# Kernel optimization log

Measured on AMD Instinct MI355X. Metric: run time of the kernel, lower is better.

The kernel has to match this reference:

```python
import jax, jax.numpy as jnp
import numpy as np
from math import sqrt

B, L, D_MODEL = 4, 128, 256
V, D_WORD = 50257, 768
H = 8  # n_heads; d_keys = D_MODEL // H = 32


def setup_inputs() -> dict:
    key = jax.random.key(0)
    ks = jax.random.split(key, 10)
    s = lambda k, shape, fan: jax.random.normal(k, shape, dtype=jnp.float32) / np.sqrt(fan)
    return {
        "time_series_embedding": jax.random.normal(ks[0], (B, L, D_MODEL), dtype=jnp.float32),
        "word_embedding": jax.random.normal(ks[1], (V, D_WORD), dtype=jnp.float32) * 0.02,
        "Wq": s(ks[2], (D_MODEL, D_MODEL), D_MODEL),
        "bq": jnp.zeros((D_MODEL,), jnp.float32),
        "Wk": s(ks[3], (D_WORD, D_MODEL), D_WORD),
        "bk": jnp.zeros((D_MODEL,), jnp.float32),
        "Wv": s(ks[4], (D_WORD, D_MODEL), D_WORD),
        "bv": jnp.zeros((D_MODEL,), jnp.float32),
        "Wo": s(ks[5], (D_MODEL, D_MODEL), D_MODEL),
        "bo": jnp.zeros((D_MODEL,), jnp.float32),
    }


def reference(time_series_embedding, word_embedding, Wq, bq, Wk, bk, Wv, bv, Wo, bo):
    b, l, _ = time_series_embedding.shape
    v, _ = word_embedding.shape
    h = H
    e = D_MODEL // h
    # projections
    query = (time_series_embedding @ Wq + bq).reshape(b, l, h, e)   # [B,L,H,E]
    key = (word_embedding @ Wk + bk).reshape(v, h, e)               # [V,H,E]
    value = (word_embedding @ Wv + bv).reshape(v, h, e)             # [V,H,E]
    scale = 1.0 / sqrt(e)
    # scores over full vocab: [B,H,V,L]
    scores = jnp.einsum('blhe,vhe->bhvl', query, key)
    # NOTE: faithful to source -- softmax over the LAST axis (l, the query dim)
    attn = jax.nn.softmax(scale * scores, axis=-1)
    # dropout is identity in eval mode
    reprog = jnp.einsum('bhvl,vhe->blhe', attn, value).reshape(b, l, h * e)
    return reprog @ Wo + bo  # [B,L,d_model]
```

## Files before the change

kernel.cpp:

```cpp
#include <hip/hip_runtime.h>
#include <hip/hip_bf16.h>
#include <string.h>

#define BB 4
#define LL 128
#define DM 256
#define VV 50257
#define VPAD 50304
#define DW 768
#define HH 8
#define EE 32

typedef __attribute__((ext_vector_type(8))) short sh8;
typedef __attribute__((ext_vector_type(4))) short sh4;
typedef __attribute__((ext_vector_type(4))) float f32x4;

static __device__ inline unsigned short bfbits(float x) {
  __hip_bfloat16 h = __float2bfloat16(x);
  unsigned short u;
  __builtin_memcpy(&u, &h, 2);
  return u;
}

#define GLDS16(gsrc, ldst)                                                    \
  __builtin_amdgcn_global_load_lds(                                          \
      (const __attribute__((address_space(1))) void*)(gsrc),                 \
      (__attribute__((address_space(3))) void*)(ldst), 16, 0, 0)

#define WAIT_VM(N)                                                           \
  __builtin_amdgcn_sched_barrier(0);                                         \
  asm volatile("s_waitcnt vmcnt(" #N ")" ::: "memory");                      \
  __builtin_amdgcn_sched_barrier(0)
#define WAIT_LGKM0                                                           \
  asm volatile("s_waitcnt lgkmcnt(0)" ::: "memory");                         \
  __builtin_amdgcn_sched_barrier(0)
#define SBARRIER                                                             \
  __builtin_amdgcn_sched_barrier(0);                                         \
  __builtin_amdgcn_s_barrier();                                              \
  __builtin_amdgcn_sched_barrier(0)

#if __has_builtin(__builtin_amdgcn_mfma_f32_16x16x16bf16_1k)
#define MFMA16(A, B, C) __builtin_amdgcn_mfma_f32_16x16x16bf16_1k(A, B, C, 0, 0, 0)
#elif __has_builtin(__builtin_amdgcn_mfma_f32_16x16x16_bf16)
#define MFMA16(A, B, C) __builtin_amdgcn_mfma_f32_16x16x16_bf16(A, B, C, 0, 0, 0)
#else
static __device__ inline f32x4 mfma16_asm(sh4 a, sh4 b, f32x4 c) {
  asm volatile("v_mfma_f32_16x16x16_bf16 %0, %1, %2, %0"
               : "+v"(c) : "v"(a), "v"(b));
  return c;
}
#define MFMA16(A, B, C) mfma16_asm(A, B, C)
#endif

__global__ __launch_bounds__(256) void prep_kernel(
    const float* __restrict__ Wk, const float* __restrict__ Wv,
    unsigned short* __restrict__ Wkt, unsigned short* __restrict__ Wvt,
    const float* __restrict__ tse, const float* __restrict__ Wq,
    const float* __restrict__ bq, unsigned short* __restrict__ Qb) {
  __shared__ float tileS[64][65];
  int bid = blockIdx.x;
  int t = threadIdx.x;
  if (bid < 96) {
    int z = bid / 48, rem = bid - z * 48;
    int x = rem % 12, y = rem / 12;
    const float* src = z ? Wv : Wk;
    unsigned short* dst = z ? Wvt : Wkt;
    int k0 = x * 64, n0 = y * 64;
    int c = t & 63, rb = t >> 6;
#pragma unroll
    for (int j = 0; j < 16; ++j) {
      int r = j * 4 + rb;
      tileS[r][c] = src[(size_t)(k0 + r) * DM + n0 + c];
    }
    __syncthreads();
#pragma unroll
    for (int j = 0; j < 16; ++j) {
      int r = j * 4 + rb;
      dst[(size_t)(n0 + r) * DW + k0 + c] = bfbits(tileS[c][r]);
    }
  } else {
    int r = bid - 96;
    int n = t;
    float* row = &tileS[0][0];
    row[n] = tse[r * DM + n];
    __syncthreads();
    float acc = bq[n];
#pragma unroll 8
    for (int k = 0; k < DM; ++k)
      acc = fmaf(row[k], Wq[k * DM + n], acc);
    const float scale = 0.17677669529663687f * 1.4426950408889634f;
    Qb[r * DM + n] = bfbits(acc * scale);
  }
}

__global__ __launch_bounds__(256, 2) void kvproj_kernel(
    const float* __restrict__ WE, const unsigned short* __restrict__ Wkt,
    const unsigned short* __restrict__ Wvt, const float* __restrict__ bk,
    const float* __restrict__ bv, unsigned short* __restrict__ Kb,
    unsigned short* __restrict__ Vbt) {
  __shared__ float WEf[2][128 * 32];
  __shared__ short Kbuf[2][128 * 32];
  __shared__ short Vbuf[2][128 * 32];

  int bx = blockIdx.x;
  int v0 = (bx >> 1) * 128;
  int colbase = (bx & 1) * 128;
  int t = threadIdx.x;
  int w = t >> 6, lane = t & 63, a = lane & 15, quad = lane >> 4;
  int wm = w >> 1, wn = w & 1;

  auto stage = [&](int kt, int p) {
#pragma unroll
    for (int i = 0; i < 4; ++i) {
      int s = w * 256 + i * 64 + lane;
      int row = s >> 3;
      int cc = (s & 7) ^ (row & 7);
      int grow = v0 + row;
      if (grow > VV - 1) grow = VV - 1;
      GLDS16(WE + (size_t)grow * DW + kt * 32 + cc * 4,
             &WEf[p][(w * 256 + i * 64) * 4]);
    }
#pragma unroll
    for (int i = 0; i < 2; ++i) {
      int s = w * 128 + i * 64 + lane;
      int row = s >> 2;
      int cc = (s & 3) ^ ((row >> 1) & 3);
      GLDS16(Wkt + (size_t)(colbase + row) * DW + kt * 32 + cc * 8,
             &Kbuf[p][(w * 128 + i * 64) * 8]);
      GLDS16(Wvt + (size_t)(colbase + row) * DW + kt * 32 + cc * 8,
             &Vbuf[p][(w * 128 + i * 64) * 8]);
    }
  };

  f32x4 Ck[4][4], Cv[4][4];
#pragma unroll
  for (int mb = 0; mb < 4; ++mb)
#pragma unroll
    for (int nb = 0; nb < 4; ++nb) {
      Ck[mb][nb] = (f32x4){0.f, 0.f, 0.f, 0.f};
      Cv[mb][nb] = (f32x4){0.f, 0.f, 0.f, 0.f};
    }

  stage(0, 0);
  stage(1, 1);

  for (int kt = 0; kt < 24; ++kt) {
    int p = kt & 1;
    if (kt < 23) {
      WAIT_VM(8);
    } else {
      WAIT_VM(0);
    }
    SBARRIER;

    sh8 A[4], Bk[4], Bv[4];
#pragma unroll
    for (int mb = 0; mb < 4; ++mb) {
      int row = wm * 64 + mb * 16 + a;
      const float* rp = &WEf[p][row * 32];
      f32x4 lo = *(const f32x4*)(rp + ((2 * quad) ^ (a & 7)) * 4);
      f32x4 hi = *(const f32x4*)(rp + ((2 * quad + 1) ^ (a & 7)) * 4);
      sh4 l4 = {(short)bfbits(lo[0]), (short)bfbits(lo[1]),
                (short)bfbits(lo[2]), (short)bfbits(lo[3])};
      sh4 h4 = {(short)bfbits(hi[0]), (short)bfbits(hi[1]),
                (short)bfbits(hi[2]), (short)bfbits(hi[3])};
      A[mb] = __builtin_shufflevector(l4, h4, 0, 1, 2, 3, 4, 5, 6, 7);
    }
#pragma unroll
    for (int nb = 0; nb < 4; ++nb) {
      int krow = (wn * 4 + nb) * 16 + a;
      int cp = (quad ^ ((krow >> 1) & 3)) * 8;
      Bk[nb] = *(const sh8*)&Kbuf[p][krow * 32 + cp];
      Bv[nb] = *(const sh8*)&Vbuf[p][krow * 32 + cp];
    }
#pragma unroll
    for (int mb = 0; mb < 4; ++mb)
#pragma unroll
      for (int nb = 0; nb < 4; ++nb) {
        Ck[mb][nb] = __builtin_amdgcn_mfma_f32_16x16x32_bf16(
            A[mb], Bk[nb], Ck[mb][nb], 0, 0, 0);
        Cv[mb][nb] = __builtin_amdgcn_mfma_f32_16x16x32_bf16(
            A[mb], Bv[nb], Cv[mb][nb], 0, 0, 0);
      }

    WAIT_LGKM0;
    SBARRIER;
    if (kt < 22) stage(kt + 2, p);
  }

  float bkv[4], bvv[4];
#pragma unroll
  for (int nb = 0; nb < 4; ++nb) {
    int n = colbase + (wn * 4 + nb) * 16 + a;
    bkv[nb] = bk[n];
    bvv[nb] = bv[n];
  }
#pragma unroll
  for (int mb = 0; mb < 4; ++mb)
#pragma unroll
    for (int nb = 0; nb < 4; ++nb) {
      int m0 = v0 + wm * 64 + mb * 16 + quad * 4;
      int n = colbase + (wn * 4 + nb) * 16 + a;
      sh4 vq;
#pragma unroll
      for (int r = 0; r < 4; ++r) {
        int m = m0 + r;
        bool ok = m < VV;
        Kb[(size_t)m * DM + n] = ok ? bfbits(Ck[mb][nb][r] + bkv[nb]) : 0;
        vq[r] = ok ? (short)bfbits(Cv[mb][nb][r] + bvv[nb]) : (short)0;
      }
      *(sh4*)&Vbt[(size_t)n * VPAD + m0] = vq;
    }
}

__global__ __launch_bounds__(256) void attn_kernel(
    const unsigned short* __restrict__ Qb, const unsigned short* __restrict__ Kb,
    const unsigned short* __restrict__ Vbt, float* __restrict__ part, int bpb,
    int nc) {
  __shared__ float Cred[4][32][129];

  int bh = blockIdx.x / bpb;
  int chunk = blockIdx.x - bh * bpb;
  int b = bh >> 3, h = bh & 7;
  int t = threadIdx.x;
  int w = t >> 6;
  int lane = t & 63;
  int a = lane & 15;
  int quad = lane >> 4;

  sh8 qf[8];
  const unsigned short* qbase = Qb + (size_t)(b * LL) * DM + h * EE;
#pragma unroll
  for (int tau = 0; tau < 8; ++tau)
    qf[tau] = *(const sh8*)(qbase + (size_t)(tau * 16 + a) * DM + quad * 8);

  f32x4 C2[2][8];
#pragma unroll
  for (int nb = 0; nb < 2; ++nb)
#pragma unroll
    for (int tau = 0; tau < 8; ++tau)
      C2[nb][tau] = (f32x4){0.f, 0.f, 0.f, 0.f};

  const int ntiles = VPAD >> 6;

  sh8 af;
  sh4 av[2];
  {
    int v0 = chunk << 6;
    af = *(const sh8*)(Kb + (size_t)(v0 + 16 * w + a) * DM + h * EE + quad * 8);
#pragma unroll
    for (int nb = 0; nb < 2; ++nb)
      av[nb] = *(const sh4*)(Vbt + (size_t)(h * EE + nb * 16 + a) * VPAD +
                             v0 + 16 * w + quad * 4);
  }

  for (int tile = chunk; tile < ntiles; tile += bpb) {
    f32x4 S[8];
#pragma unroll
    for (int tau = 0; tau < 8; ++tau) {
      f32x4 z = {0.f, 0.f, 0.f, 0.f};
      S[tau] = __builtin_amdgcn_mfma_f32_16x16x32_bf16(af, qf[tau], z, 0, 0, 0);
    }

    sh8 af2 = af;
    sh4 av2[2] = {av[0], av[1]};
    int nt = tile + bpb;
    if (nt < ntiles) {
      int v0n = nt << 6;
      af2 = *(const sh8*)(Kb + (size_t)(v0n + 16 * w + a) * DM + h * EE + quad * 8);
#pragma unroll
      for (int nb = 0; nb < 2; ++nb)
        av2[nb] = *(const sh4*)(Vbt + (size_t)(h * EE + nb * 16 + a) * VPAD +
                                v0n + 16 * w + quad * 4);
    }

    float sm[4], inv[4];
#pragma unroll
    for (int r = 0; r < 4; ++r) sm[r] = 0.f;
#pragma unroll
    for (int tau = 0; tau < 8; ++tau)
#pragma unroll
      for (int r = 0; r < 4; ++r) {
        float ex = __builtin_amdgcn_exp2f(S[tau][r]);
        S[tau][r] = ex;
        sm[r] += ex;
      }
#pragma unroll
    for (int msk = 1; msk <= 8; msk <<= 1)
#pragma unroll
      for (int r = 0; r < 4; ++r)
        sm[r] += __shfl_xor(sm[r], msk);
#pragma unroll
    for (int r = 0; r < 4; ++r) inv[r] = 1.f / sm[r];

    sh4 pb[8];
#pragma unroll
    for (int tau = 0; tau < 8; ++tau) {
      pb[tau][0] = (short)bfbits(S[tau][0] * inv[0]);
      pb[tau][1] = (short)bfbits(S[tau][1] * inv[1]);
      pb[tau][2] = (short)bfbits(S[tau][2] * inv[2]);
      pb[tau][3] = (short)bfbits(S[tau][3] * inv[3]);
    }

#pragma unroll
    for (int nb = 0; nb < 2; ++nb)
#pragma unroll
      for (int tau = 0; tau < 8; ++tau)
        C2[nb][tau] = MFMA16(av[nb], pb[tau], C2[nb][tau]);

    af = af2;
    av[0] = av2[0];
    av[1] = av2[1];
  }

#pragma unroll
  for (int nb = 0; nb < 2; ++nb)
#pragma unroll
    for (int tau = 0; tau < 8; ++tau)
#pragma unroll
      for (int r = 0; r < 4; ++r)
        Cred[w][nb * 16 + quad * 4 + r][tau * 16 + a] = C2[nb][tau][r];
  __syncthreads();
#pragma unroll
  for (int j = 0; j < 16; ++j) {
    int f = t + 256 * j;
    int e = f & 31, l = f >> 5;
    float s = Cred[0][e][l] + Cred[1][e][l] + Cred[2][e][l] + Cred[3][e][l];
    size_t idx = (size_t)(b * LL + l) * DM + h * EE + e;
    if (nc > 1)
      part[(size_t)chunk * (BB * LL * DM) + idx] = s;
    else
      atomicAdd(&part[idx], s);
  }
}

__global__ __launch_bounds__(256) void outproj_kernel(
    const float* __restrict__ part, const float* __restrict__ Wo,
    const float* __restrict__ bo, float* __restrict__ out, int nc) {
  __shared__ float row[DM];
  int r = blockIdx.x, n = threadIdx.x;
  float s = 0.f;
  for (int c = 0; c < nc; ++c)
    s += part[(size_t)c * (BB * LL * DM) + (size_t)r * DM + n];
  row[n] = s;
  __syncthreads();
  float acc = bo[n];
#pragma unroll 8
  for (int k = 0; k < DM; ++k)
    acc = fmaf(row[k], Wo[k * DM + n], acc);
  out[r * DM + n] = acc;
}

extern "C" void kernel_launch(void* const* d_in, const int* in_sizes, int n_in,
                              void* d_out, int out_size, void* d_ws, size_t ws_size,
                              hipStream_t stream) {
  const float* tse = (const float*)d_in[0];
  const float* WE  = (const float*)d_in[1];
  const float* Wq  = (const float*)d_in[2];
  const float* bq  = (const float*)d_in[3];
  const float* Wk  = (const float*)d_in[4];
  const float* bk  = (const float*)d_in[5];
  const float* Wv  = (const float*)d_in[6];
  const float* bv  = (const float*)d_in[7];
  const float* Wo  = (const float*)d_in[8];
  const float* bo  = (const float*)d_in[9];
  float* out = (float*)d_out;

  char* ws = (char*)d_ws;
  const size_t QB_BYTES   = (size_t)BB * LL * DM * 2;
  const size_t KV_BYTES   = (size_t)VPAD * DM * 2;
  const size_t WT_BYTES   = (size_t)DM * DW * 2;
  const size_t PART_BYTES = (size_t)BB * LL * DM * 4;
  unsigned short* Qb  = (unsigned short*)ws;
  unsigned short* Kb  = (unsigned short*)(ws + QB_BYTES);
  unsigned short* Vbt = (unsigned short*)(ws + QB_BYTES + KV_BYTES);
  char* X = ws + QB_BYTES + 2 * KV_BYTES;
  unsigned short* Wkt = (unsigned short*)X;
  unsigned short* Wvt = (unsigned short*)(X + WT_BYTES);
  float* part = (float*)X;

  const int BPB = 32;

  const size_t NEED_PART =
      QB_BYTES + 2 * KV_BYTES + (size_t)BPB * PART_BYTES;
  const int nc = (ws_size >= NEED_PART) ? BPB : 1;

  prep_kernel<<<96 + BB * LL, 256, 0, stream>>>(Wk, Wv, Wkt, Wvt, tse, Wq, bq, Qb);
  kvproj_kernel<<<(VPAD / 128) * 2, 256, 0, stream>>>(WE, Wkt, Wvt, bk, bv, Kb, Vbt);
  if (nc == 1)
    (void)hipMemsetAsync(part, 0, PART_BYTES, stream);
  attn_kernel<<<32 * BPB, 256, 0, stream>>>(Qb, Kb, Vbt, part, BPB, nc);
  outproj_kernel<<<BB * LL, 256, 0, stream>>>(part, Wo, bo, out, nc);
}
```

Baseline: 408.7 us.

## Pre-convert word embedding to tiled bf16 and use 16x16x32 MFMA KV projection

The prep kernel gains extra blocks that convert the fp32 word embedding into a bf16 layout tiled by 32-column k-slices. A new KV projection kernel then streams those bf16 tiles straight into LDS with swizzling and uses 16x16x32 bf16 MFMAs at higher occupancy. This is meant to cut LDS footprint and conversion work inside the GEMM, at the cost of an extra full read and write of the embedding matrix. The attention reduction also shrinks its LDS buffer by having half the waves accumulate into the other half's slots, which adds one extra barrier.

```diff
diff --git a/kernel.cpp b/kernel.cpp
--- a/kernel.cpp
+++ b/kernel.cpp
@@ -56,7 +56,8 @@
     const float* __restrict__ Wk, const float* __restrict__ Wv,
     unsigned short* __restrict__ Wkt, unsigned short* __restrict__ Wvt,
     const float* __restrict__ tse, const float* __restrict__ Wq,
-    const float* __restrict__ bq, unsigned short* __restrict__ Qb) {
+    const float* __restrict__ bq, unsigned short* __restrict__ Qb,
+    const float* __restrict__ WE, unsigned short* __restrict__ WEbt) {
   __shared__ float tileS[64][65];
   int bid = blockIdx.x;
   int t = threadIdx.x;
@@ -78,7 +79,7 @@
       int r = j * 4 + rb;
       dst[(size_t)(n0 + r) * DW + k0 + c] = bfbits(tileS[c][r]);
     }
-  } else {
+  } else if (bid < 608) {
     int r = bid - 96;
     int n = t;
     float* row = &tileS[0][0];
@@ -90,10 +91,135 @@
       acc = fmaf(row[k], Wq[k * DM + n], acc);
     const float scale = 0.17677669529663687f * 1.4426950408889634f;
     Qb[r * DM + n] = bfbits(acc * scale);
-  }
-}
-
-__global__ __launch_bounds__(256, 2) void kvproj_kernel(
+  } else {
+    int v0 = (bid - 608) * 64;
+    int c4 = (t & 7) * 4;
+    int r0 = t >> 3;
+#pragma unroll 4
+    for (int kt = 0; kt < 24; ++kt)
+#pragma unroll
+      for (int g = 0; g < 2; ++g) {
+        int row = v0 + g * 32 + r0;
+        sh4 o = {0, 0, 0, 0};
+        if (row < VV) {
+          f32x4 f = *(const f32x4*)(WE + (size_t)row * DW + kt * 32 + c4);
+          o[0] = (short)bfbits(f[0]);
+          o[1] = (short)bfbits(f[1]);
+          o[2] = (short)bfbits(f[2]);
+          o[3] = (short)bfbits(f[3]);
+        }
+        *(sh4*)&WEbt[((size_t)kt * VPAD + row) * 32 + c4] = o;
+      }
+  }
+}
+
+__global__ __launch_bounds__(256, 3) void kvproj_bf16t(
+    const unsigned short* __restrict__ WEbt, const unsigned short* __restrict__ Wkt,
+    const unsigned short* __restrict__ Wvt, const float* __restrict__ bk,
+    const float* __restrict__ bv, unsigned short* __restrict__ Kb,
+    unsigned short* __restrict__ Vbt) {
+  __shared__ short WEb[2][128 * 32];
+  __shared__ short Kbuf[2][128 * 32];
+  __shared__ short Vbuf[2][128 * 32];
+
+  int bx = blockIdx.x;
+  int v0 = (bx >> 1) * 128;
+  int colbase = (bx & 1) * 128;
+  int t = threadIdx.x;
+  int w = t >> 6, lane = t & 63, a = lane & 15, quad = lane >> 4;
+  int wm = w >> 1, wn = w & 1;
+
+  auto stage = [&](int kt, int p) {
+#pragma unroll
+    for (int i = 0; i < 2; ++i) {
+      int s = w * 128 + i * 64 + lane;
+      int row = s >> 2;
+      int cc = (s & 3) ^ ((row >> 1) & 3);
+      GLDS16(WEbt + ((size_t)kt * VPAD + v0 + row) * 32 + cc * 8,
+             &WEb[p][(w * 128 + i * 64) * 8]);
+      GLDS16(Wkt + (size_t)(colbase + row) * DW + kt * 32 + cc * 8,
+             &Kbuf[p][(w * 128 + i * 64) * 8]);
+      GLDS16(Wvt + (size_t)(colbase + row) * DW + kt * 32 + cc * 8,
+             &Vbuf[p][(w * 128 + i * 64) * 8]);
+    }
+  };
+
+  f32x4 Ck[4][4], Cv[4][4];
+#pragma unroll
+  for (int mb = 0; mb < 4; ++mb)
+#pragma unroll
+    for (int nb = 0; nb < 4; ++nb) {
+      Ck[mb][nb] = (f32x4){0.f, 0.f, 0.f, 0.f};
+      Cv[mb][nb] = (f32x4){0.f, 0.f, 0.f, 0.f};
+    }
+
+  stage(0, 0);
+  stage(1, 1);
+
+  for (int kt = 0; kt < 24; ++kt) {
+    int p = kt & 1;
+    if (kt < 23) {
+      WAIT_VM(6);
+    } else {
+      WAIT_VM(0);
+    }
+    SBARRIER;
+
+    sh8 A[4], Bk[4], Bv[4];
+#pragma unroll
+    for (int mb = 0; mb < 4; ++mb) {
+      int row = wm * 64 + mb * 16 + a;
+      int cp = (quad ^ ((row >> 1) & 3)) * 8;
+      A[mb] = *(const sh8*)&WEb[p][row * 32 + cp];
+    }
+#pragma unroll
+    for (int nb = 0; nb < 4; ++nb) {
+      int krow = (wn * 4 + nb) * 16 + a;
+      int cp = (quad ^ ((krow >> 1) & 3)) * 8;
+      Bk[nb] = *(const sh8*)&Kbuf[p][krow * 32 + cp];
+      Bv[nb] = *(const sh8*)&Vbuf[p][krow * 32 + cp];
+    }
+#pragma unroll
+    for (int mb = 0; mb < 4; ++mb)
+#pragma unroll
+      for (int nb = 0; nb < 4; ++nb) {
+        Ck[mb][nb] = __builtin_amdgcn_mfma_f32_16x16x32_bf16(
+            A[mb], Bk[nb], Ck[mb][nb], 0, 0, 0);
+        Cv[mb][nb] = __builtin_amdgcn_mfma_f32_16x16x32_bf16(
+            A[mb], Bv[nb], Cv[mb][nb], 0, 0, 0);
+      }
+
+    WAIT_LGKM0;
+    SBARRIER;
+    if (kt < 22) stage(kt + 2, p);
+  }
+
+  float bkv[4], bvv[4];
+#pragma unroll
+  for (int nb = 0; nb < 4; ++nb) {
+    int n = colbase + (wn * 4 + nb) * 16 + a;
+    bkv[nb] = bk[n];
+    bvv[nb] = bv[n];
+  }
+#pragma unroll
+  for (int mb = 0; mb < 4; ++mb)
+#pragma unroll
+    for (int nb = 0; nb < 4; ++nb) {
+      int m0 = v0 + wm * 64 + mb * 16 + quad * 4;
+      int n = colbase + (wn * 4 + nb) * 16 + a;
+      sh4 vq;
+#pragma unroll
+      for (int r = 0; r < 4; ++r) {
+        int m = m0 + r;
+        bool ok = m < VV;
+        Kb[(size_t)m * DM + n] = ok ? bfbits(Ck[mb][nb][r] + bkv[nb]) : 0;
+        vq[r] = ok ? (short)bfbits(Cv[mb][nb][r] + bvv[nb]) : (short)0;
+      }
+      *(sh4*)&Vbt[(size_t)n * VPAD + m0] = vq;
+    }
+}
+
+__global__ __launch_bounds__(256, 2) void kvproj_fp32(
     const float* __restrict__ WE, const unsigned short* __restrict__ Wkt,
     const unsigned short* __restrict__ Wvt, const float* __restrict__ bk,
     const float* __restrict__ bv, unsigned short* __restrict__ Kb,
@@ -217,7 +343,7 @@
     const unsigned short* __restrict__ Qb, const unsigned short* __restrict__ Kb,
     const unsigned short* __restrict__ Vbt, float* __restrict__ part, int bpb,
     int nc) {
-  __shared__ float Cred[4][32][129];
+  __shared__ float Cred[2][32][129];
 
   int bh = blockIdx.x / bpb;
   int chunk = blockIdx.x - bh * bpb;
@@ -313,19 +439,31 @@
     av[1] = av2[1];
   }
 
-#pragma unroll
-  for (int nb = 0; nb < 2; ++nb)
-#pragma unroll
-    for (int tau = 0; tau < 8; ++tau)
-#pragma unroll
-      for (int r = 0; r < 4; ++r)
-        Cred[w][nb * 16 + quad * 4 + r][tau * 16 + a] = C2[nb][tau][r];
+  if (w < 2) {
+#pragma unroll
+    for (int nb = 0; nb < 2; ++nb)
+#pragma unroll
+      for (int tau = 0; tau < 8; ++tau)
+#pragma unroll
+        for (int r = 0; r < 4; ++r)
+          Cred[w][nb * 16 + quad * 4 + r][tau * 16 + a] = C2[nb][tau][r];
+  }
+  __syncthreads();
+  if (w >= 2) {
+#pragma unroll
+    for (int nb = 0; nb < 2; ++nb)
+#pragma unroll
+      for (int tau = 0; tau < 8; ++tau)
+#pragma unroll
+        for (int r = 0; r < 4; ++r)
+          Cred[w - 2][nb * 16 + quad * 4 + r][tau * 16 + a] += C2[nb][tau][r];
+  }
   __syncthreads();
 #pragma unroll
   for (int j = 0; j < 16; ++j) {
     int f = t + 256 * j;
     int e = f & 31, l = f >> 5;
-    float s = Cred[0][e][l] + Cred[1][e][l] + Cred[2][e][l] + Cred[3][e][l];
+    float s = Cred[0][e][l] + Cred[1][e][l];
     size_t idx = (size_t)(b * LL + l) * DM + h * EE + e;
     if (nc > 1)
       part[(size_t)chunk * (BB * LL * DM) + idx] = s;
@@ -370,23 +508,33 @@
   const size_t QB_BYTES   = (size_t)BB * LL * DM * 2;
   const size_t KV_BYTES   = (size_t)VPAD * DM * 2;
   const size_t WT_BYTES   = (size_t)DM * DW * 2;
+  const size_t WEBT_BYTES = (size_t)VPAD * DW * 2;
   const size_t PART_BYTES = (size_t)BB * LL * DM * 4;
   unsigned short* Qb  = (unsigned short*)ws;
   unsigned short* Kb  = (unsigned short*)(ws + QB_BYTES);
   unsigned short* Vbt = (unsigned short*)(ws + QB_BYTES + KV_BYTES);
   char* X = ws + QB_BYTES + 2 * KV_BYTES;
-  unsigned short* Wkt = (unsigned short*)X;
-  unsigned short* Wvt = (unsigned short*)(X + WT_BYTES);
+  unsigned short* Wkt  = (unsigned short*)X;
+  unsigned short* Wvt  = (unsigned short*)(X + WT_BYTES);
+  unsigned short* WEbt = (unsigned short*)(X + 2 * WT_BYTES);
   float* part = (float*)X;
 
   const int BPB = 32;
 
-  const size_t NEED_PART =
-      QB_BYTES + 2 * KV_BYTES + (size_t)BPB * PART_BYTES;
+  const size_t BASE = QB_BYTES + 2 * KV_BYTES;
+  const size_t NEED_TILED = BASE + 2 * WT_BYTES + WEBT_BYTES;
+  const size_t NEED_PART  = BASE + (size_t)BPB * PART_BYTES;
+  const bool tiled = (ws_size >= NEED_TILED);
   const int nc = (ws_size >= NEED_PART) ? BPB : 1;
 
-  prep_kernel<<<96 + BB * LL, 256, 0, stream>>>(Wk, Wv, Wkt, Wvt, tse, Wq, bq, Qb);
-  kvproj_kernel<<<(VPAD / 128) * 2, 256, 0, stream>>>(WE, Wkt, Wvt, bk, bv, Kb, Vbt);
+  prep_kernel<<<tiled ? 1394 : 608, 256, 0, stream>>>(
+      Wk, Wv, Wkt, Wvt, tse, Wq, bq, Qb, WE, WEbt);
+  if (tiled)
+    kvproj_bf16t<<<(VPAD / 128) * 2, 256, 0, stream>>>(WEbt, Wkt, Wvt, bk, bv,
+                                                       Kb, Vbt);
+  else
+    kvproj_fp32<<<(VPAD / 128) * 2, 256, 0, stream>>>(WE, Wkt, Wvt, bk, bv,
+                                                      Kb, Vbt);
   if (nc == 1)
     (void)hipMemsetAsync(part, 0, PART_BYTES, stream);
   attn_kernel<<<32 * BPB, 256, 0, stream>>>(Qb, Kb, Vbt, part, BPB, nc);
```

Measured after the change: 554.0 us. 35.6% more time.

## Split kvproj WE tile into half-buffers and halve attn reduction LDS

Applied to the files above, without the earlier changes.

The kvproj kernel now stages the fp32 word-embedding tile as two 64-row halves instead of a double-buffered 128-row tile. The first half's MFMAs overlap the load of the second half, and the next step's first half is prefetched while the second half computes. This cuts LDS use so occupancy can rise to 3 blocks per CU, traded against tighter waits and more barriers per k-step. Separately, the attention kernel's cross-wave reduction buffer shrinks from 4 to 2 slices by adding in place in two phases, which lowers LDS footprint at the cost of an extra barrier.

```diff
diff --git a/kernel.cpp b/kernel.cpp
--- a/kernel.cpp
+++ b/kernel.cpp
@@ -93,12 +93,12 @@
   }
 }
 
-__global__ __launch_bounds__(256, 2) void kvproj_kernel(
+__global__ __launch_bounds__(256, 3) void kvproj_kernel(
     const float* __restrict__ WE, const unsigned short* __restrict__ Wkt,
     const unsigned short* __restrict__ Wvt, const float* __restrict__ bk,
     const float* __restrict__ bv, unsigned short* __restrict__ Kb,
     unsigned short* __restrict__ Vbt) {
-  __shared__ float WEf[2][128 * 32];
+  __shared__ float WEh[2][64 * 32];
   __shared__ short Kbuf[2][128 * 32];
   __shared__ short Vbuf[2][128 * 32];
 
@@ -109,26 +109,29 @@
   int w = t >> 6, lane = t & 63, a = lane & 15, quad = lane >> 4;
   int wm = w >> 1, wn = w & 1;
 
-  auto stage = [&](int kt, int p) {
-#pragma unroll
-    for (int i = 0; i < 4; ++i) {
-      int s = w * 256 + i * 64 + lane;
-      int row = s >> 3;
-      int cc = (s & 7) ^ (row & 7);
-      int grow = v0 + row;
+  auto stageWEh = [&](int kt, int h) {
+#pragma unroll
+    for (int i = 0; i < 2; ++i) {
+      int s = w * 128 + i * 64 + lane;
+      int rho = s >> 3;
+      int cc = (s & 7) ^ (rho & 7);
+      int g = (rho < 32) ? (h * 32 + rho) : (64 + h * 32 + (rho - 32));
+      int grow = v0 + g;
       if (grow > VV - 1) grow = VV - 1;
       GLDS16(WE + (size_t)grow * DW + kt * 32 + cc * 4,
-             &WEf[p][(w * 256 + i * 64) * 4]);
-    }
+             &WEh[h][(w * 128 + i * 64) * 4]);
+    }
+  };
+  auto stageKV = [&](int kt, int pb) {
 #pragma unroll
     for (int i = 0; i < 2; ++i) {
       int s = w * 128 + i * 64 + lane;
       int row = s >> 2;
       int cc = (s & 3) ^ ((row >> 1) & 3);
       GLDS16(Wkt + (size_t)(colbase + row) * DW + kt * 32 + cc * 8,
-             &Kbuf[p][(w * 128 + i * 64) * 8]);
+             &Kbuf[pb][(w * 128 + i * 64) * 8]);
       GLDS16(Wvt + (size_t)(colbase + row) * DW + kt * 32 + cc * 8,
-             &Vbuf[p][(w * 128 + i * 64) * 8]);
+             &Vbuf[pb][(w * 128 + i * 64) * 8]);
     }
   };
 
@@ -141,51 +144,85 @@
       Cv[mb][nb] = (f32x4){0.f, 0.f, 0.f, 0.f};
     }
 
-  stage(0, 0);
-  stage(1, 1);
+  stageWEh(0, 0);
+  stageKV(0, 0);
+  stageWEh(0, 1);
+  stageKV(1, 1);
 
   for (int kt = 0; kt < 24; ++kt) {
-    int p = kt & 1;
-    if (kt < 23) {
-      WAIT_VM(8);
+    int pb = kt & 1;
+
+    if (kt == 0) {
+      WAIT_VM(6);
     } else {
       WAIT_VM(0);
     }
     SBARRIER;
-
-    sh8 A[4], Bk[4], Bv[4];
-#pragma unroll
-    for (int mb = 0; mb < 4; ++mb) {
-      int row = wm * 64 + mb * 16 + a;
-      const float* rp = &WEf[p][row * 32];
+    if (kt > 0) stageWEh(kt, 1);
+
+    sh8 A0[2], Bk[4], Bv[4];
+#pragma unroll
+    for (int mu = 0; mu < 2; ++mu) {
+      int rho = wm * 32 + mu * 16 + a;
+      const float* rp = &WEh[0][rho * 32];
       f32x4 lo = *(const f32x4*)(rp + ((2 * quad) ^ (a & 7)) * 4);
       f32x4 hi = *(const f32x4*)(rp + ((2 * quad + 1) ^ (a & 7)) * 4);
       sh4 l4 = {(short)bfbits(lo[0]), (short)bfbits(lo[1]),
                 (short)bfbits(lo[2]), (short)bfbits(lo[3])};
       sh4 h4 = {(short)bfbits(hi[0]), (short)bfbits(hi[1]),
                 (short)bfbits(hi[2]), (short)bfbits(hi[3])};
-      A[mb] = __builtin_shufflevector(l4, h4, 0, 1, 2, 3, 4, 5, 6, 7);
+      A0[mu] = __builtin_shufflevector(l4, h4, 0, 1, 2, 3, 4, 5, 6, 7);
     }
 #pragma unroll
     for (int nb = 0; nb < 4; ++nb) {
       int krow = (wn * 4 + nb) * 16 + a;
       int cp = (quad ^ ((krow >> 1) & 3)) * 8;
-      Bk[nb] = *(const sh8*)&Kbuf[p][krow * 32 + cp];
-      Bv[nb] = *(const sh8*)&Vbuf[p][krow * 32 + cp];
-    }
-#pragma unroll
-    for (int mb = 0; mb < 4; ++mb)
+      Bk[nb] = *(const sh8*)&Kbuf[pb][krow * 32 + cp];
+      Bv[nb] = *(const sh8*)&Vbuf[pb][krow * 32 + cp];
+    }
+#pragma unroll
+    for (int mu = 0; mu < 2; ++mu)
 #pragma unroll
       for (int nb = 0; nb < 4; ++nb) {
-        Ck[mb][nb] = __builtin_amdgcn_mfma_f32_16x16x32_bf16(
-            A[mb], Bk[nb], Ck[mb][nb], 0, 0, 0);
-        Cv[mb][nb] = __builtin_amdgcn_mfma_f32_16x16x32_bf16(
-            A[mb], Bv[nb], Cv[mb][nb], 0, 0, 0);
+        Ck[mu][nb] = __builtin_amdgcn_mfma_f32_16x16x32_bf16(
+            A0[mu], Bk[nb], Ck[mu][nb], 0, 0, 0);
+        Cv[mu][nb] = __builtin_amdgcn_mfma_f32_16x16x32_bf16(
+            A0[mu], Bv[nb], Cv[mu][nb], 0, 0, 0);
       }
 
-    WAIT_LGKM0;
+    if (kt == 0) {
+      WAIT_VM(4);
+    } else {
+      WAIT_VM(0);
+    }
     SBARRIER;
-    if (kt < 22) stage(kt + 2, p);
+    if (kt < 23) {
+      stageWEh(kt + 1, 0);
+      if (kt > 0) stageKV(kt + 1, pb ^ 1);
+    }
+
+    sh8 A1[2];
+#pragma unroll
+    for (int mu = 0; mu < 2; ++mu) {
+      int rho = wm * 32 + mu * 16 + a;
+      const float* rp = &WEh[1][rho * 32];
+      f32x4 lo = *(const f32x4*)(rp + ((2 * quad) ^ (a & 7)) * 4);
+      f32x4 hi = *(const f32x4*)(rp + ((2 * quad + 1) ^ (a & 7)) * 4);
+      sh4 l4 = {(short)bfbits(lo[0]), (short)bfbits(lo[1]),
+                (short)bfbits(lo[2]), (short)bfbits(lo[3])};
+      sh4 h4 = {(short)bfbits(hi[0]), (short)bfbits(hi[1]),
+                (short)bfbits(hi[2]), (short)bfbits(hi[3])};
+      A1[mu] = __builtin_shufflevector(l4, h4, 0, 1, 2, 3, 4, 5, 6, 7);
+    }
+#pragma unroll
+    for (int mu = 0; mu < 2; ++mu)
+#pragma unroll
+      for (int nb = 0; nb < 4; ++nb) {
+        Ck[2 + mu][nb] = __builtin_amdgcn_mfma_f32_16x16x32_bf16(
+            A1[mu], Bk[nb], Ck[2 + mu][nb], 0, 0, 0);
+        Cv[2 + mu][nb] = __builtin_amdgcn_mfma_f32_16x16x32_bf16(
+            A1[mu], Bv[nb], Cv[2 + mu][nb], 0, 0, 0);
+      }
   }
 
   float bkv[4], bvv[4];
@@ -199,7 +236,8 @@
   for (int mb = 0; mb < 4; ++mb)
 #pragma unroll
     for (int nb = 0; nb < 4; ++nb) {
-      int m0 = v0 + wm * 64 + mb * 16 + quad * 4;
+      int h = mb >> 1, mu = mb & 1;
+      int m0 = v0 + wm * 64 + h * 32 + mu * 16 + quad * 4;
       int n = colbase + (wn * 4 + nb) * 16 + a;
       sh4 vq;
 #pragma unroll
@@ -217,7 +255,7 @@
     const unsigned short* __restrict__ Qb, const unsigned short* __restrict__ Kb,
     const unsigned short* __restrict__ Vbt, float* __restrict__ part, int bpb,
     int nc) {
-  __shared__ float Cred[4][32][129];
+  __shared__ float Cred[2][32][129];
 
   int bh = blockIdx.x / bpb;
   int chunk = blockIdx.x - bh * bpb;
@@ -313,19 +351,31 @@
     av[1] = av2[1];
   }
 
-#pragma unroll
-  for (int nb = 0; nb < 2; ++nb)
-#pragma unroll
-    for (int tau = 0; tau < 8; ++tau)
-#pragma unroll
-      for (int r = 0; r < 4; ++r)
-        Cred[w][nb * 16 + quad * 4 + r][tau * 16 + a] = C2[nb][tau][r];
+  if (w < 2) {
+#pragma unroll
+    for (int nb = 0; nb < 2; ++nb)
+#pragma unroll
+      for (int tau = 0; tau < 8; ++tau)
+#pragma unroll
+        for (int r = 0; r < 4; ++r)
+          Cred[w][nb * 16 + quad * 4 + r][tau * 16 + a] = C2[nb][tau][r];
+  }
+  __syncthreads();
+  if (w >= 2) {
+#pragma unroll
+    for (int nb = 0; nb < 2; ++nb)
+#pragma unroll
+      for (int tau = 0; tau < 8; ++tau)
+#pragma unroll
+        for (int r = 0; r < 4; ++r)
+          Cred[w - 2][nb * 16 + quad * 4 + r][tau * 16 + a] += C2[nb][tau][r];
+  }
   __syncthreads();
 #pragma unroll
   for (int j = 0; j < 16; ++j) {
     int f = t + 256 * j;
     int e = f & 31, l = f >> 5;
-    float s = Cred[0][e][l] + Cred[1][e][l] + Cred[2][e][l] + Cred[3][e][l];
+    float s = Cred[0][e][l] + Cred[1][e][l];
     size_t idx = (size_t)(b * LL + l) * DM + h * EE + e;
     if (nc > 1)
       part[(size_t)chunk * (BB * LL * DM) + idx] = s;
```

Result: slower. 624.7 us (+52.9%).

## Store K head-major and halve attention reduction shared memory

Applied to the files above, without the earlier changes.

The K projection output is now stored head-major ([H][VPAD][E]), so each attention block reads contiguous 64-byte rows for its head instead of 64-byte pieces strided by 512 bytes. This should improve K load coalescing in the attention kernel. The kvproj store for K becomes more scattered, since each element goes to a per-head plane. The cross-wave reduction now uses two LDS buffers with an extra barrier and accumulate step, cutting LDS use from about 66KB to 33KB so more blocks can be resident.

```diff
diff --git a/kernel.cpp b/kernel.cpp
--- a/kernel.cpp
+++ b/kernel.cpp
@@ -96,7 +96,7 @@
 __global__ __launch_bounds__(256, 2) void kvproj_kernel(
     const float* __restrict__ WE, const unsigned short* __restrict__ Wkt,
     const unsigned short* __restrict__ Wvt, const float* __restrict__ bk,
-    const float* __restrict__ bv, unsigned short* __restrict__ Kb,
+    const float* __restrict__ bv, unsigned short* __restrict__ Kbh,
     unsigned short* __restrict__ Vbt) {
   __shared__ float WEf[2][128 * 32];
   __shared__ short Kbuf[2][128 * 32];
@@ -201,12 +201,14 @@
     for (int nb = 0; nb < 4; ++nb) {
       int m0 = v0 + wm * 64 + mb * 16 + quad * 4;
       int n = colbase + (wn * 4 + nb) * 16 + a;
+      int hh = n >> 5, e = n & 31;
       sh4 vq;
 #pragma unroll
       for (int r = 0; r < 4; ++r) {
         int m = m0 + r;
         bool ok = m < VV;
-        Kb[(size_t)m * DM + n] = ok ? bfbits(Ck[mb][nb][r] + bkv[nb]) : 0;
+        Kbh[((size_t)hh * VPAD + m) * EE + e] =
+            ok ? bfbits(Ck[mb][nb][r] + bkv[nb]) : 0;
         vq[r] = ok ? (short)bfbits(Cv[mb][nb][r] + bvv[nb]) : (short)0;
       }
       *(sh4*)&Vbt[(size_t)n * VPAD + m0] = vq;
@@ -214,10 +216,10 @@
 }
 
 __global__ __launch_bounds__(256) void attn_kernel(
-    const unsigned short* __restrict__ Qb, const unsigned short* __restrict__ Kb,
+    const unsigned short* __restrict__ Qb, const unsigned short* __restrict__ Kbh,
     const unsigned short* __restrict__ Vbt, float* __restrict__ part, int bpb,
     int nc) {
-  __shared__ float Cred[4][32][129];
+  __shared__ float Cred[2][32][129];
 
   int bh = blockIdx.x / bpb;
   int chunk = blockIdx.x - bh * bpb;
@@ -228,6 +230,8 @@
   int a = lane & 15;
   int quad = lane >> 4;
 
+  const unsigned short* Kh = Kbh + (size_t)h * VPAD * EE;
+
   sh8 qf[8];
   const unsigned short* qbase = Qb + (size_t)(b * LL) * DM + h * EE;
 #pragma unroll
@@ -247,7 +251,7 @@
   sh4 av[2];
   {
     int v0 = chunk << 6;
-    af = *(const sh8*)(Kb + (size_t)(v0 + 16 * w + a) * DM + h * EE + quad * 8);
+    af = *(const sh8*)(Kh + (size_t)(v0 + 16 * w + a) * EE + quad * 8);
 #pragma unroll
     for (int nb = 0; nb < 2; ++nb)
       av[nb] = *(const sh4*)(Vbt + (size_t)(h * EE + nb * 16 + a) * VPAD +
@@ -267,7 +271,7 @@
     int nt = tile + bpb;
     if (nt < ntiles) {
       int v0n = nt << 6;
-      af2 = *(const sh8*)(Kb + (size_t)(v0n + 16 * w + a) * DM + h * EE + quad * 8);
+      af2 = *(const sh8*)(Kh + (size_t)(v0n + 16 * w + a) * EE + quad * 8);
 #pragma unroll
       for (int nb = 0; nb < 2; ++nb)
         av2[nb] = *(const sh4*)(Vbt + (size_t)(h * EE + nb * 16 + a) * VPAD +
@@ -313,19 +317,31 @@
     av[1] = av2[1];
   }
 
-#pragma unroll
-  for (int nb = 0; nb < 2; ++nb)
-#pragma unroll
-    for (int tau = 0; tau < 8; ++tau)
-#pragma unroll
-      for (int r = 0; r < 4; ++r)
-        Cred[w][nb * 16 + quad * 4 + r][tau * 16 + a] = C2[nb][tau][r];
+  if (w < 2) {
+#pragma unroll
+    for (int nb = 0; nb < 2; ++nb)
+#pragma unroll
+      for (int tau = 0; tau < 8; ++tau)
+#pragma unroll
+        for (int r = 0; r < 4; ++r)
+          Cred[w][nb * 16 + quad * 4 + r][tau * 16 + a] = C2[nb][tau][r];
+  }
+  __syncthreads();
+  if (w >= 2) {
+#pragma unroll
+    for (int nb = 0; nb < 2; ++nb)
+#pragma unroll
+      for (int tau = 0; tau < 8; ++tau)
+#pragma unroll
+        for (int r = 0; r < 4; ++r)
+          Cred[w - 2][nb * 16 + quad * 4 + r][tau * 16 + a] += C2[nb][tau][r];
+  }
   __syncthreads();
 #pragma unroll
   for (int j = 0; j < 16; ++j) {
     int f = t + 256 * j;
     int e = f & 31, l = f >> 5;
-    float s = Cred[0][e][l] + Cred[1][e][l] + Cred[2][e][l] + Cred[3][e][l];
+    float s = Cred[0][e][l] + Cred[1][e][l];
     size_t idx = (size_t)(b * LL + l) * DM + h * EE + e;
     if (nc > 1)
       part[(size_t)chunk * (BB * LL * DM) + idx] = s;
@@ -372,7 +388,7 @@
   const size_t WT_BYTES   = (size_t)DM * DW * 2;
   const size_t PART_BYTES = (size_t)BB * LL * DM * 4;
   unsigned short* Qb  = (unsigned short*)ws;
-  unsigned short* Kb  = (unsigned short*)(ws + QB_BYTES);
+  unsigned short* Kbh = (unsigned short*)(ws + QB_BYTES);
   unsigned short* Vbt = (unsigned short*)(ws + QB_BYTES + KV_BYTES);
   char* X = ws + QB_BYTES + 2 * KV_BYTES;
   unsigned short* Wkt = (unsigned short*)X;
@@ -386,9 +402,9 @@
   const int nc = (ws_size >= NEED_PART) ? BPB : 1;
 
   prep_kernel<<<96 + BB * LL, 256, 0, stream>>>(Wk, Wv, Wkt, Wvt, tse, Wq, bq, Qb);
-  kvproj_kernel<<<(VPAD / 128) * 2, 256, 0, stream>>>(WE, Wkt, Wvt, bk, bv, Kb, Vbt);
+  kvproj_kernel<<<(VPAD / 128) * 2, 256, 0, stream>>>(WE, Wkt, Wvt, bk, bv, Kbh, Vbt);
   if (nc == 1)
     (void)hipMemsetAsync(part, 0, PART_BYTES, stream);
-  attn_kernel<<<32 * BPB, 256, 0, stream>>>(Qb, Kb, Vbt, part, BPB, nc);
+  attn_kernel<<<32 * BPB, 256, 0, stream>>>(Qb, Kbh, Vbt, part, BPB, nc);
   outproj_kernel<<<BB * LL, 256, 0, stream>>>(part, Wo, bo, out, nc);
 }
```

Result: no change. 409.4 us (+0.2%).
